# Optimization experiments

Measured on AMD Instinct MI355X. Metric: run time of the kernel, lower is better.

Reference implementation:

```python
import jax, jax.numpy as jnp
import numpy as np

N, E, G = 20000, 640000, 64
D_IN, H, C, D_OUT = 256, 4, 64, 32
HC = H * C


def gat_layer(x, W, a_src, a_dst, b, src, dst, n_nodes, heads, ch):
    # x: [N, F_in], W: [F_in, H*C]
    h = (x @ W).reshape(n_nodes, heads, ch)          # [N,H,C]
    es = jnp.einsum('nhc,hc->nh', h, a_src)          # [N,H]
    ed = jnp.einsum('nhc,hc->nh', h, a_dst)
    e = jax.nn.leaky_relu(es[src] + ed[dst], 0.2)    # [Etot,H]
    m = jax.ops.segment_max(e, dst, num_segments=n_nodes)
    m = jnp.where(jnp.isfinite(m), m, 0.0)
    ex = jnp.exp(e - m[dst])
    denom = jax.ops.segment_sum(ex, dst, num_segments=n_nodes)
    alpha = ex / jnp.maximum(denom[dst], 1e-16)      # softmax over in-edges per dst
    out = jax.ops.segment_sum(alpha[:, :, None] * h[src], dst, num_segments=n_nodes)
    return out.reshape(n_nodes, heads * ch) + b


def setup_inputs() -> dict:
    key = jax.random.key(0)
    ks = jax.random.split(key, 14)
    g1 = 1.0 / np.sqrt(D_IN)
    g2 = 1.0 / np.sqrt(HC)
    inp = {
        'x': jax.random.normal(ks[0], (N, D_IN), jnp.float32),
        'edge_index': jax.random.randint(ks[1], (2, E), 0, N, jnp.int64 if jax.config.jax_enable_x64 else jnp.int32),
        'batch': jnp.sort(jax.random.randint(ks[2], (N,), 0, G)),
        'W1': jax.random.normal(ks[3], (D_IN, HC), jnp.float32) * g1,
        'a_src1': jax.random.normal(ks[4], (H, C), jnp.float32) * g2,
        'a_dst1': jax.random.normal(ks[5], (H, C), jnp.float32) * g2,
        'b1': jnp.zeros((HC,), jnp.float32),
        'W2': jax.random.normal(ks[6], (HC, HC), jnp.float32) * g2,
        'a_src2': jax.random.normal(ks[7], (H, C), jnp.float32) * g2,
        'a_dst2': jax.random.normal(ks[8], (H, C), jnp.float32) * g2,
        'b2': jnp.zeros((HC,), jnp.float32),
        'Wp': jax.random.normal(ks[9], (HC, D_OUT), jnp.float32) * g2,
        'bp': jnp.zeros((D_OUT,), jnp.float32),
    }
    return inp


def reference(x, edge_index, batch, W1, a_src1, a_dst1, b1, W2, a_src2, a_dst2, b2, Wp, bp):
    # add self-loops (PyG GATConv default)
    loop = jnp.arange(N, dtype=edge_index.dtype)
    src = jnp.concatenate([edge_index[0], loop])
    dst = jnp.concatenate([edge_index[1], loop])
    x1 = jax.nn.relu(gat_layer(x, W1, a_src1, a_dst1, b1, src, dst, N, H, C))
    # dropout p=0.6 is identity in eval mode
    x2 = jax.nn.relu(gat_layer(x1, W2, a_src2, a_dst2, b2, src, dst, N, H, C))
    node_scores = x2 @ Wp + bp                        # [N, D_OUT]
    sums = jax.ops.segment_sum(node_scores, batch, num_segments=G)
    counts = jax.ops.segment_sum(jnp.ones((N,), node_scores.dtype), batch, num_segments=G)
    return sums / jnp.maximum(counts, 1.0)[:, None]   # [G, D_OUT]
```

## Files before the change

kernel.cpp:

```cpp
#include <hip/hip_runtime.h>
#include <hip/hip_bf16.h>
#include <cstdint>

#define NNODES 20000
#define NEDGES 640000
#define ETOT   (NEDGES + NNODES)
#define NGROUP 64
#define HC     256
#define DOUT   32
#define EBLK   5120
#define NBLK   (NEDGES / EBLK)
#define CBLK   ((NNODES + 255) / 256)

typedef short bf16x8 __attribute__((ext_vector_type(8)));
typedef short s16x4  __attribute__((ext_vector_type(4)));
typedef float f32x4  __attribute__((ext_vector_type(4)));
typedef float f32x2  __attribute__((ext_vector_type(2)));
typedef int   s32x4  __attribute__((ext_vector_type(4)));
typedef unsigned int u32x4 __attribute__((ext_vector_type(4)));

__device__ __forceinline__ float b2f(__hip_bfloat16 v) { return __bfloat162float(v); }
__device__ __forceinline__ float bs2f(short v) {
    union { unsigned int u; float f; } c; c.u = ((unsigned int)(unsigned short)v) << 16; return c.f;
}
__device__ __forceinline__ short f2bs(float v) {
    __hip_bfloat16 b = __float2bfloat16(v);
    union { __hip_bfloat16 b; short s; } u; u.b = b; return u.s;
}
__device__ __forceinline__ float ldf(const void* __restrict__ p, size_t i, int bf) {
    return bf ? __bfloat162float(((const __hip_bfloat16*)p)[i]) : ((const float*)p)[i];
}
__device__ __forceinline__ int ld_idx(const int* __restrict__ p, size_t i, int f64) {
    return f64 ? p[2 * i] : p[i];
}

__global__ void k_probe(const unsigned int* __restrict__ xw, const int* __restrict__ ei,
                        int* __restrict__ flag, float* __restrict__ sx, int* __restrict__ cnt) {
    int t = threadIdx.x;
    for (int i = t; i < NGROUP * HC; i += 256) sx[i] = 0.f;
    if (t < NGROUP) cnt[t] = 0;
    if (t < 64) {
        int l = t;
        int ones = 0, zeros = 0;
#pragma unroll
        for (int r = 0; r < 4; r++) {
            unsigned long long b1 = __ballot((xw[r * 64 + l] >> 14) & 1);
            unsigned long long b2 = __ballot(ei[2 * (r * 64 + l) + 1] == 0);
            ones  += __popcll(b1);
            zeros += __popcll(b2);
        }
        if (l == 0) { flag[1] = (ones < 64) ? 1 : 0; flag[0] = (zeros > 200) ? 1 : 0; }
    }
}

__global__ __launch_bounds__(256) void k_lhist(const int* __restrict__ ei,
                                               int* __restrict__ H,
                                               const int* __restrict__ flag) {
    __shared__ int hl[NNODES];
    int t = threadIdx.x, b = blockIdx.x, f = flag[0];
    s32x4* hl4 = reinterpret_cast<s32x4*>(hl);
    for (int i = t; i < NNODES / 4; i += 256) hl4[i] = (s32x4){0, 0, 0, 0};
    __syncthreads();
    int s0 = b * EBLK;
    if (f) {
        const int* d64 = ei + 2 * NEDGES;
        for (int i0 = s0; i0 < s0 + EBLK; i0 += 512) {
            int i = i0 + 2 * t;
            s32x4 v = *reinterpret_cast<const s32x4*>(d64 + 2 * (size_t)i);
            atomicAdd(&hl[v[0]], 1);
            atomicAdd(&hl[v[2]], 1);
        }
    } else {
        const int* d32 = ei + NEDGES;
        for (int i0 = s0; i0 < s0 + EBLK; i0 += 1024) {
            int i = i0 + 4 * t;
            s32x4 v = *reinterpret_cast<const s32x4*>(d32 + i);
            atomicAdd(&hl[v[0]], 1); atomicAdd(&hl[v[1]], 1);
            atomicAdd(&hl[v[2]], 1); atomicAdd(&hl[v[3]], 1);
        }
    }
    __syncthreads();
    s32x4* Hb4 = reinterpret_cast<s32x4*>(H + (size_t)b * NNODES);
    for (int i = t; i < NNODES / 4; i += 256) Hb4[i] = hl4[i];
}

__global__ __launch_bounds__(256) void k_colsum(const int* __restrict__ H,
                                                int* __restrict__ deg,
                                                int* __restrict__ bsum) {
    __shared__ int wred[4];
    int t = threadIdx.x, n = blockIdx.x * 256 + t;
    int s = 0;
    if (n < NNODES) {
#pragma unroll 5
        for (int b = 0; b < NBLK; b++) s += H[(size_t)b * NNODES + n];
        s += 1;
        deg[n] = s;
    }
    int r = s;
#pragma unroll
    for (int o = 1; o < 64; o <<= 1) r += __shfl_xor(r, o);
    if ((t & 63) == 0) wred[t >> 6] = r;
    __syncthreads();
    if (t == 0) bsum[blockIdx.x] = wred[0] + wred[1] + wred[2] + wred[3];
}

__global__ void k_scansm(const int* __restrict__ bsum, int* __restrict__ boff,
                         int* __restrict__ off) {
    __shared__ int w0tot;
    int t = threadIdx.x, lane = t & 63, w = t >> 6;
    int v = (t < CBLK) ? bsum[t] : 0;
    int sc = v;
#pragma unroll
    for (int o = 1; o < 64; o <<= 1) {
        int u = __shfl_up(sc, o);
        if (lane >= o) sc += u;
    }
    if (w == 0 && lane == 63) w0tot = sc;
    __syncthreads();
    int excl = sc - v + (w ? w0tot : 0);
    if (t < CBLK) boff[t] = excl;
    if (t == 0) off[NNODES] = ETOT;
}

__global__ __launch_bounds__(256) void k_base(int* __restrict__ H,
                                              const int* __restrict__ deg,
                                              const int* __restrict__ boff,
                                              int* __restrict__ off,
                                              int* __restrict__ csr) {
    __shared__ int wtot[4];
    int t = threadIdx.x, blk = blockIdx.x;
    int n = blk * 256 + t;
    int d = (n < NNODES) ? deg[n] : 0;
    int lane = t & 63, w = t >> 6;
    int sc = d;
#pragma unroll
    for (int o = 1; o < 64; o <<= 1) {
        int u = __shfl_up(sc, o);
        if (lane >= o) sc += u;
    }
    if (lane == 63) wtot[w] = sc;
    __syncthreads();
    int woff = 0;
    for (int i = 0; i < w; i++) woff += wtot[i];
    int excl = woff + sc - d;
    if (n < NNODES) {
        int o0 = boff[blk] + excl;
        off[n] = o0;
        csr[o0] = n;
        int run = o0 + 1;
#pragma unroll 5
        for (int b = 0; b < NBLK; b++) {
            size_t idx = (size_t)b * NNODES + n;
            int tt = H[idx];
            H[idx] = run;
            run += tt;
        }
    }
}

__global__ __launch_bounds__(256) void k_scatter2(const int* __restrict__ ei,
                                                  const int* __restrict__ H,
                                                  int* __restrict__ csr,
                                                  const int* __restrict__ flag) {
    __shared__ int base_l[NNODES];
    int t = threadIdx.x, b = blockIdx.x, f = flag[0];
    const s32x4* Hb4 = reinterpret_cast<const s32x4*>(H + (size_t)b * NNODES);
    s32x4* bl4 = reinterpret_cast<s32x4*>(base_l);
    for (int i = t; i < NNODES / 4; i += 256) bl4[i] = Hb4[i];
    __syncthreads();
    int s0 = b * EBLK;
    if (f) {
        const int* d64 = ei + 2 * NEDGES;
        for (int i0 = s0; i0 < s0 + EBLK; i0 += 512) {
            int i = i0 + 2 * t;
            s32x4 sv = *reinterpret_cast<const s32x4*>(ei + 2 * (size_t)i);
            s32x4 dv = *reinterpret_cast<const s32x4*>(d64 + 2 * (size_t)i);
            int p0 = atomicAdd(&base_l[dv[0]], 1);
            csr[p0] = sv[0];
            int p1 = atomicAdd(&base_l[dv[2]], 1);
            csr[p1] = sv[2];
        }
    } else {
        const int* d32 = ei + NEDGES;
        for (int i0 = s0; i0 < s0 + EBLK; i0 += 1024) {
            int i = i0 + 4 * t;
            s32x4 sv = *reinterpret_cast<const s32x4*>(ei + i);
            s32x4 dv = *reinterpret_cast<const s32x4*>(d32 + i);
#pragma unroll
            for (int k = 0; k < 4; k++) {
                int p = atomicAdd(&base_l[dv[k]], 1);
                csr[p] = sv[k];
            }
        }
    }
}

__global__ void k_wt(const void* __restrict__ W1, const void* __restrict__ W2,
                     __hip_bfloat16* __restrict__ Wt1, __hip_bfloat16* __restrict__ Wt2,
                     const int* __restrict__ flag) {
    int i = blockIdx.x * 256 + threadIdx.x;
    int which = i >> 16;
    int j = i & 65535;
    int k = j >> 8, n = j & 255;
    const void* W = which ? W2 : W1;
    __hip_bfloat16* Wt = which ? Wt2 : Wt1;
    Wt[(size_t)n * 256 + k] = __float2bfloat16(ldf(W, (size_t)k * 256 + n, flag[1]));
}

__global__ __launch_bounds__(256) void k_gemm(const void* __restrict__ A,
                                              const __hip_bfloat16* __restrict__ Bt,
                                              __hip_bfloat16* __restrict__ Hout,
                                              const void* __restrict__ a_src,
                                              const void* __restrict__ a_dst,
                                              float* __restrict__ es4, float* __restrict__ ed4,
                                              const int* __restrict__ flag, int force_bf) {
    int bf   = flag[1];
    int abf  = force_bf | bf;
    int w    = threadIdx.x >> 6;
    int lane = threadIdx.x & 63;
    int mr   = lane & 15;
    int quad = lane >> 4;
    int r0   = blockIdx.x * 16;
    if (r0 >= NNODES) return;
    f32x4 acc[4];
#pragma unroll
    for (int j = 0; j < 4; j++) acc[j] = (f32x4){0.f, 0.f, 0.f, 0.f};
    size_t rowoff = (size_t)(r0 + mr) * HC;
    const __hip_bfloat16* Btw = Bt + (size_t)w * 64 * HC;
    for (int kk = 0; kk < HC; kk += 32) {
        bf16x8 a;
        if (abf) {
            a = *reinterpret_cast<const bf16x8*>((const __hip_bfloat16*)A + rowoff + kk + quad * 8);
        } else {
            const float* af = (const float*)A + rowoff + kk + quad * 8;
            f32x4 lo = *reinterpret_cast<const f32x4*>(af);
            f32x4 hi = *reinterpret_cast<const f32x4*>(af + 4);
#pragma unroll
            for (int ii = 0; ii < 4; ii++) { a[ii] = f2bs(lo[ii]); a[ii + 4] = f2bs(hi[ii]); }
        }
#pragma unroll
        for (int j = 0; j < 4; j++) {
            bf16x8 b = *reinterpret_cast<const bf16x8*>(Btw + (size_t)(j * 16 + mr) * HC + kk + quad * 8);
            acc[j] = __builtin_amdgcn_mfma_f32_16x16x32_bf16(a, b, acc[j], 0, 0, 0);
        }
    }
#pragma unroll
    for (int j = 0; j < 4; j++)
#pragma unroll
        for (int r = 0; r < 4; r++)
            Hout[(size_t)(r0 + quad * 4 + r) * HC + w * 64 + j * 16 + mr] = __float2bfloat16(acc[j][r]);
    float ps[4] = {0.f, 0.f, 0.f, 0.f}, pd[4] = {0.f, 0.f, 0.f, 0.f};
#pragma unroll
    for (int j = 0; j < 4; j++) {
        float asv = ldf(a_src, (size_t)(w * 64 + j * 16 + mr), bf);
        float adv = ldf(a_dst, (size_t)(w * 64 + j * 16 + mr), bf);
#pragma unroll
        for (int r = 0; r < 4; r++) {
            ps[r] = fmaf(acc[j][r], asv, ps[r]);
            pd[r] = fmaf(acc[j][r], adv, pd[r]);
        }
    }
#pragma unroll
    for (int o = 1; o < 16; o <<= 1)
#pragma unroll
        for (int r = 0; r < 4; r++) {
            ps[r] += __shfl_xor(ps[r], o);
            pd[r] += __shfl_xor(pd[r], o);
        }
    if (mr == 0)
#pragma unroll
        for (int r = 0; r < 4; r++) {
            int row = r0 + quad * 4 + r;
            es4[(size_t)row * 4 + w] = ps[r];
            ed4[(size_t)row * 4 + w] = pd[r];
        }
}

__global__ __launch_bounds__(256) void k_agg(const __hip_bfloat16* __restrict__ Hb,
                                             const float* __restrict__ es4, const float* __restrict__ ed4,
                                             const void* __restrict__ bias,
                                             const int* __restrict__ off, const int* __restrict__ csr,
                                             const int* __restrict__ flag,
                                             __hip_bfloat16* __restrict__ out) {
    __shared__ float p_lds[4][4][64];
    __shared__ int   s_lds[4][64];
    int wv = threadIdx.x >> 6;
    int l  = threadIdx.x & 63;
    int half = l >> 5;
    int hl   = l & 31;
    int hd8  = hl >> 3;
    int bf = flag[1];
    int n0 = blockIdx.x * 4 + wv;
    for (int n = n0; n < NNODES; n += 10000) {
        int base = off[n], deg = off[n + 1] - base;
        f32x4 edv = *reinterpret_cast<const f32x4*>(ed4 + (size_t)n * 4);
        f32x4 m    = (f32x4){-INFINITY, -INFINITY, -INFINITY, -INFINITY};
        f32x4 dsum = (f32x4){0.f, 0.f, 0.f, 0.f};
        f32x2 acc2[4];
#pragma unroll
        for (int d = 0; d < 4; d++) acc2[d] = (f32x2){0.f, 0.f};
        for (int c0 = 0; c0 < deg; c0 += 64) {
            int cn = min(deg - c0, 64);
            int s = 0;
            f32x4 ev;
            if (l < cn) {
                s = csr[base + c0 + l];
                f32x4 e = *reinterpret_cast<const f32x4*>(es4 + (size_t)s * 4);
#pragma unroll
                for (int h = 0; h < 4; h++) {
                    float t = e[h] + edv[h];
                    ev[h] = (t > 0.f) ? t : 0.2f * t;
                }
            } else {
#pragma unroll
                for (int h = 0; h < 4; h++) ev[h] = -INFINITY;
            }
            s_lds[wv][l] = s;
            f32x4 mc = ev;
#pragma unroll
            for (int o = 32; o; o >>= 1)
#pragma unroll
                for (int h = 0; h < 4; h++) mc[h] = fmaxf(mc[h], __shfl_xor(mc[h], o));
            f32x4 al, pv;
#pragma unroll
            for (int h = 0; h < 4; h++) {
                float nm = fmaxf(m[h], mc[h]);
                al[h] = __expf(m[h] - nm);
                m[h]  = nm;
            }
#pragma unroll
            for (int h = 0; h < 4; h++) pv[h] = (l < cn) ? __expf(ev[h] - m[h]) : 0.f;
            f32x4 sc = pv;
#pragma unroll
            for (int o = 32; o; o >>= 1)
#pragma unroll
                for (int h = 0; h < 4; h++) sc[h] += __shfl_xor(sc[h], o);
#pragma unroll
            for (int h = 0; h < 4; h++) dsum[h] = dsum[h] * al[h] + sc[h];
            float a8 = al[hd8];
#pragma unroll
            for (int d = 0; d < 4; d++) acc2[d] *= a8;
#pragma unroll
            for (int h = 0; h < 4; h++) p_lds[wv][h][l] = pv[h];
            int jn = (cn + 15) & ~15;
            for (int j = 0; j < jn; j += 16) {
                int e0 = j + 8 * half;
                s32x4 sA = *reinterpret_cast<const s32x4*>(&s_lds[wv][e0]);
                s32x4 sB = *reinterpret_cast<const s32x4*>(&s_lds[wv][e0 + 4]);
                f32x4 pA = *reinterpret_cast<const f32x4*>(&p_lds[wv][hd8][e0]);
                f32x4 pB = *reinterpret_cast<const f32x4*>(&p_lds[wv][hd8][e0 + 4]);
                u32x4 hv[8];
#pragma unroll
                for (int i = 0; i < 8; i++) {
                    int sj = (i < 4) ? sA[i & 3] : sB[i & 3];
                    hv[i] = *reinterpret_cast<const u32x4*>(Hb + (size_t)sj * HC + hl * 8);
                }
#pragma unroll
                for (int i = 0; i < 8; i++) {
                    float p = (i < 4) ? pA[i & 3] : pB[i & 3];
#pragma unroll
                    for (int d = 0; d < 4; d++) {
                        unsigned int u = hv[i][d];
                        f32x2 h2;
                        h2.x = __uint_as_float(u << 16);
                        h2.y = __uint_as_float(u & 0xFFFF0000u);
                        acc2[d] += h2 * p;
                    }
                }
            }
        }
#pragma unroll
        for (int d = 0; d < 4; d++) {
            acc2[d].x += __shfl_xor(acc2[d].x, 32);
            acc2[d].y += __shfl_xor(acc2[d].y, 32);
        }
        float rinv = 1.0f / fmaxf(dsum[hd8], 1e-16f);
        if (half == 0) {
            bf16x8 ov;
#pragma unroll
            for (int d = 0; d < 4; d++) {
                float v0 = acc2[d].x * rinv + ldf(bias, (size_t)hl * 8 + 2 * d, bf);
                float v1 = acc2[d].y * rinv + ldf(bias, (size_t)hl * 8 + 2 * d + 1, bf);
                ov[2 * d]     = f2bs(fmaxf(v0, 0.f));
                ov[2 * d + 1] = f2bs(fmaxf(v1, 0.f));
            }
            *reinterpret_cast<bf16x8*>(out + (size_t)n * HC + hl * 8) = ov;
        }
    }
}

__global__ __launch_bounds__(256) void k_groupsum(const __hip_bfloat16* __restrict__ X2,
                                                  const int* __restrict__ batch,
                                                  float* __restrict__ sx, int* __restrict__ cnt,
                                                  const int* __restrict__ flag) {
    const int RPB = NNODES / 250;
    int b = blockIdx.x, f = flag[0];
    int sub = threadIdx.x >> 6, l = threadIdx.x & 63;
    int r = b * RPB + sub;
    f32x4 acc = (f32x4){0.f, 0.f, 0.f, 0.f};
    int curg = ld_idx(batch, r, f);
    int cacc = 0;
    for (int k = 0; k < RPB / 4; k++, r += 4) {
        int g = ld_idx(batch, r, f);
        if (g != curg) {
#pragma unroll
            for (int c = 0; c < 4; c++) atomicAdd(&sx[(size_t)curg * HC + l * 4 + c], acc[c]);
            if (l == 0) atomicAdd(&cnt[curg], cacc);
            acc = (f32x4){0.f, 0.f, 0.f, 0.f}; cacc = 0; curg = g;
        }
        s16x4 hv = *reinterpret_cast<const s16x4*>(X2 + (size_t)r * HC + l * 4);
#pragma unroll
        for (int c = 0; c < 4; c++) acc[c] += bs2f(hv[c]);
        cacc++;
    }
#pragma unroll
    for (int c = 0; c < 4; c++) atomicAdd(&sx[(size_t)curg * HC + l * 4 + c], acc[c]);
    if (l == 0) atomicAdd(&cnt[curg], cacc);
}

__global__ __launch_bounds__(256) void k_final(const float* __restrict__ sx,
                                               const void* __restrict__ Wp,
                                               const void* __restrict__ bp,
                                               const int* __restrict__ cnt,
                                               const int* __restrict__ flag,
                                               void* __restrict__ out) {
    __shared__ float red[8][32];
    int g = blockIdx.x, t = threadIdx.x;
    int c = t & 31, seg = t >> 5;
    int bf = flag[1];
    const float* sxg = sx + (size_t)g * HC;
    float a = 0.f;
#pragma unroll
    for (int k = 0; k < 32; k++) {
        int kk = seg * 32 + k;
        a = fmaf(sxg[kk], ldf(Wp, (size_t)kk * DOUT + c, bf), a);
    }
    red[seg][c] = a;
    __syncthreads();
    if (t < 32) {
        float s = 0.f;
#pragma unroll
        for (int i = 0; i < 8; i++) s += red[i][t];
        int ct = cnt[g];
        float v = (ct > 0) ? (s / ct + ldf(bp, (size_t)t, bf)) : 0.f;
        if (bf) ((__hip_bfloat16*)out)[g * DOUT + t] = __float2bfloat16(v);
        else    ((float*)out)[g * DOUT + t]          = v;
    }
}

extern "C" void kernel_launch(void* const* d_in, const int* in_sizes, int n_in,
                              void* d_out, int out_size, void* d_ws, size_t ws_size,
                              hipStream_t stream) {
    (void)in_sizes; (void)n_in; (void)out_size; (void)ws_size;
    const void* x   = d_in[0];
    const int*  ei  = (const int*)d_in[1];
    const int*  bat = (const int*)d_in[2];
    const void* W1  = d_in[3];
    const void* as1 = d_in[4];
    const void* ad1 = d_in[5];
    const void* b1  = d_in[6];
    const void* W2  = d_in[7];
    const void* as2 = d_in[8];
    const void* ad2 = d_in[9];
    const void* b2  = d_in[10];
    const void* Wp  = d_in[11];
    const void* bp  = d_in[12];

    char* ws = (char*)d_ws;
    size_t o = 0;
    auto alloc = [&](size_t bytes) -> char* {
        char* p = ws + o;
        o += (bytes + 255) & ~(size_t)255;
        return p;
    };
    __hip_bfloat16* hb  = (__hip_bfloat16*)alloc((size_t)NNODES * HC * 2);
    __hip_bfloat16* xb  = (__hip_bfloat16*)alloc((size_t)NNODES * HC * 2);
    __hip_bfloat16* xb2 = (__hip_bfloat16*)alloc((size_t)NNODES * HC * 2);
    __hip_bfloat16* Wt1 = (__hip_bfloat16*)alloc((size_t)HC * HC * 2);
    __hip_bfloat16* Wt2 = (__hip_bfloat16*)alloc((size_t)HC * HC * 2);
    float* es = (float*)alloc((size_t)NNODES * 4 * 4);
    float* ed = (float*)alloc((size_t)NNODES * 4 * 4);
    int* H    = (int*)alloc((size_t)NBLK * NNODES * 4);
    int* deg  = (int*)alloc((size_t)NNODES * 4);
    int* off  = (int*)alloc((size_t)(NNODES + 1) * 4);
    int* csr  = (int*)alloc((size_t)ETOT * 4);
    int* bsum = (int*)alloc((size_t)CBLK * 4);
    int* boff = (int*)alloc((size_t)CBLK * 4);
    float* sx = (float*)alloc((size_t)NGROUP * HC * 4);
    int* cnt  = (int*)alloc(256);
    int* flag = (int*)alloc(256);

    k_probe<<<1, 256, 0, stream>>>((const unsigned int*)x, ei, flag, sx, cnt);
    k_lhist<<<NBLK, 256, 0, stream>>>(ei, H, flag);
    k_colsum<<<CBLK, 256, 0, stream>>>(H, deg, bsum);
    k_scansm<<<1, 128, 0, stream>>>(bsum, boff, off);
    k_base<<<CBLK, 256, 0, stream>>>(H, deg, boff, off, csr);
    k_scatter2<<<NBLK, 256, 0, stream>>>(ei, H, csr, flag);
    k_wt<<<512, 256, 0, stream>>>(W1, W2, Wt1, Wt2, flag);

    k_gemm<<<NNODES / 16, 256, 0, stream>>>(x, Wt1, hb, as1, ad1, es, ed, flag, 0);
    k_agg<<<2500, 256, 0, stream>>>(hb, es, ed, b1, off, csr, flag, xb);

    k_gemm<<<NNODES / 16, 256, 0, stream>>>(xb, Wt2, hb, as2, ad2, es, ed, flag, 1);
    k_agg<<<2500, 256, 0, stream>>>(hb, es, ed, b2, off, csr, flag, xb2);

    k_groupsum<<<250, 256, 0, stream>>>(xb2, bat, sx, cnt, flag);
    k_final<<<NGROUP, 256, 0, stream>>>(sx, Wp, bp, cnt, flag, d_out);
}
```

Measured before the change: 299.7 us.

## Use a global score upper bound for softmax and merge the offset scan into k_base

```diff
diff --git a/kernel.cpp b/kernel.cpp
--- a/kernel.cpp
+++ b/kernel.cpp
@@ -33,12 +33,21 @@
 __device__ __forceinline__ int ld_idx(const int* __restrict__ p, size_t i, int f64) {
     return f64 ? p[2 * i] : p[i];
 }
+__device__ __forceinline__ unsigned enc_f(float f) {
+    unsigned u = __float_as_uint(f);
+    return (u >> 31) ? ~u : (u | 0x80000000u);
+}
+__device__ __forceinline__ float dec_f(unsigned e) {
+    return (e >> 31) ? __uint_as_float(e & 0x7FFFFFFFu) : __uint_as_float(~e);
+}
 
 __global__ void k_probe(const unsigned int* __restrict__ xw, const int* __restrict__ ei,
-                        int* __restrict__ flag, float* __restrict__ sx, int* __restrict__ cnt) {
+                        int* __restrict__ flag, float* __restrict__ sx, int* __restrict__ cnt,
+                        unsigned int* __restrict__ gmaxu) {
     int t = threadIdx.x;
     for (int i = t; i < NGROUP * HC; i += 256) sx[i] = 0.f;
     if (t < NGROUP) cnt[t] = 0;
+    if (t < 64) gmaxu[t] = 0x007FFFFFu;
     if (t < 64) {
         int l = t;
         int ones = 0, zeros = 0;
@@ -104,30 +113,13 @@
     if (t == 0) bsum[blockIdx.x] = wred[0] + wred[1] + wred[2] + wred[3];
 }
 
-__global__ void k_scansm(const int* __restrict__ bsum, int* __restrict__ boff,
-                         int* __restrict__ off) {
-    __shared__ int w0tot;
-    int t = threadIdx.x, lane = t & 63, w = t >> 6;
-    int v = (t < CBLK) ? bsum[t] : 0;
-    int sc = v;
-#pragma unroll
-    for (int o = 1; o < 64; o <<= 1) {
-        int u = __shfl_up(sc, o);
-        if (lane >= o) sc += u;
-    }
-    if (w == 0 && lane == 63) w0tot = sc;
-    __syncthreads();
-    int excl = sc - v + (w ? w0tot : 0);
-    if (t < CBLK) boff[t] = excl;
-    if (t == 0) off[NNODES] = ETOT;
-}
-
 __global__ __launch_bounds__(256) void k_base(int* __restrict__ H,
                                               const int* __restrict__ deg,
-                                              const int* __restrict__ boff,
+                                              const int* __restrict__ bsum,
                                               int* __restrict__ off,
                                               int* __restrict__ csr) {
     __shared__ int wtot[4];
+    __shared__ int boff_s;
     int t = threadIdx.x, blk = blockIdx.x;
     int n = blk * 256 + t;
     int d = (n < NNODES) ? deg[n] : 0;
@@ -139,12 +131,20 @@
         if (lane >= o) sc += u;
     }
     if (lane == 63) wtot[w] = sc;
+    if (w == 0) {
+        int v = (lane < blk) ? bsum[lane] : 0;
+        if (lane + 64 < blk) v += bsum[lane + 64];
+#pragma unroll
+        for (int o = 1; o < 64; o <<= 1) v += __shfl_xor(v, o);
+        if (lane == 0) boff_s = v;
+    }
     __syncthreads();
     int woff = 0;
     for (int i = 0; i < w; i++) woff += wtot[i];
     int excl = woff + sc - d;
+    if (blk == 0 && t == 0) off[NNODES] = ETOT;
     if (n < NNODES) {
-        int o0 = boff[blk] + excl;
+        int o0 = boff_s + excl;
         off[n] = o0;
         csr[o0] = n;
         int run = o0 + 1;
@@ -213,7 +213,9 @@
                                               const void* __restrict__ a_src,
                                               const void* __restrict__ a_dst,
                                               float* __restrict__ es4, float* __restrict__ ed4,
+                                              unsigned int* __restrict__ gmaxu,
                                               const int* __restrict__ flag, int force_bf) {
+    __shared__ u32x4 hst4[512];
     int bf   = flag[1];
     int abf  = force_bf | bf;
     int w    = threadIdx.x >> 6;
@@ -221,7 +223,6 @@
     int mr   = lane & 15;
     int quad = lane >> 4;
     int r0   = blockIdx.x * 16;
-    if (r0 >= NNODES) return;
     f32x4 acc[4];
 #pragma unroll
     for (int j = 0; j < 4; j++) acc[j] = (f32x4){0.f, 0.f, 0.f, 0.f};
@@ -244,11 +245,12 @@
             acc[j] = __builtin_amdgcn_mfma_f32_16x16x32_bf16(a, b, acc[j], 0, 0, 0);
         }
     }
+    short* hst = reinterpret_cast<short*>(hst4);
 #pragma unroll
     for (int j = 0; j < 4; j++)
 #pragma unroll
         for (int r = 0; r < 4; r++)
-            Hout[(size_t)(r0 + quad * 4 + r) * HC + w * 64 + j * 16 + mr] = __float2bfloat16(acc[j][r]);
+            hst[(quad * 4 + r) * HC + w * 64 + j * 16 + mr] = f2bs(acc[j][r]);
     float ps[4] = {0.f, 0.f, 0.f, 0.f}, pd[4] = {0.f, 0.f, 0.f, 0.f};
 #pragma unroll
     for (int j = 0; j < 4; j++) {
@@ -267,6 +269,10 @@
             ps[r] += __shfl_xor(ps[r], o);
             pd[r] += __shfl_xor(pd[r], o);
         }
+    float pm = fmaxf(fmaxf(ps[0], ps[1]), fmaxf(ps[2], ps[3]));
+    pm = fmaxf(pm, __shfl_xor(pm, 16));
+    pm = fmaxf(pm, __shfl_xor(pm, 32));
+    if (lane == 0) atomicMax(&gmaxu[w * 16], enc_f(pm));
     if (mr == 0)
 #pragma unroll
         for (int r = 0; r < 4; r++) {
@@ -274,12 +280,17 @@
             es4[(size_t)row * 4 + w] = ps[r];
             ed4[(size_t)row * 4 + w] = pd[r];
         }
+    __syncthreads();
+    u32x4* dst = reinterpret_cast<u32x4*>((short*)Hout + (size_t)r0 * HC);
+    dst[threadIdx.x * 2]     = hst4[threadIdx.x * 2];
+    dst[threadIdx.x * 2 + 1] = hst4[threadIdx.x * 2 + 1];
 }
 
 __global__ __launch_bounds__(256) void k_agg(const __hip_bfloat16* __restrict__ Hb,
                                              const float* __restrict__ es4, const float* __restrict__ ed4,
                                              const void* __restrict__ bias,
                                              const int* __restrict__ off, const int* __restrict__ csr,
+                                             const unsigned int* __restrict__ gmaxu,
                                              const int* __restrict__ flag,
                                              __hip_bfloat16* __restrict__ out) {
     __shared__ float p_lds[4][4][64];
@@ -290,11 +301,19 @@
     int hl   = l & 31;
     int hd8  = hl >> 3;
     int bf = flag[1];
+    f32x4 gm;
+#pragma unroll
+    for (int h = 0; h < 4; h++) gm[h] = dec_f(gmaxu[h * 16]);
     int n0 = blockIdx.x * 4 + wv;
     for (int n = n0; n < NNODES; n += 10000) {
         int base = off[n], deg = off[n + 1] - base;
         f32x4 edv = *reinterpret_cast<const f32x4*>(ed4 + (size_t)n * 4);
-        f32x4 m    = (f32x4){-INFINITY, -INFINITY, -INFINITY, -INFINITY};
+        f32x4 M;
+#pragma unroll
+        for (int h = 0; h < 4; h++) {
+            float t0 = gm[h] + edv[h];
+            M[h] = (t0 > 0.f) ? t0 : 0.2f * t0;
+        }
         f32x4 dsum = (f32x4){0.f, 0.f, 0.f, 0.f};
         f32x2 acc2[4];
 #pragma unroll
@@ -302,46 +321,22 @@
         for (int c0 = 0; c0 < deg; c0 += 64) {
             int cn = min(deg - c0, 64);
             int s = 0;
-            f32x4 ev;
+            f32x4 pv = (f32x4){0.f, 0.f, 0.f, 0.f};
             if (l < cn) {
                 s = csr[base + c0 + l];
                 f32x4 e = *reinterpret_cast<const f32x4*>(es4 + (size_t)s * 4);
 #pragma unroll
                 for (int h = 0; h < 4; h++) {
                     float t = e[h] + edv[h];
-                    ev[h] = (t > 0.f) ? t : 0.2f * t;
+                    t = (t > 0.f) ? t : 0.2f * t;
+                    pv[h] = __expf(t - M[h]);
                 }
-            } else {
-#pragma unroll
-                for (int h = 0; h < 4; h++) ev[h] = -INFINITY;
             }
             s_lds[wv][l] = s;
-            f32x4 mc = ev;
-#pragma unroll
-            for (int o = 32; o; o >>= 1)
-#pragma unroll
-                for (int h = 0; h < 4; h++) mc[h] = fmaxf(mc[h], __shfl_xor(mc[h], o));
-            f32x4 al, pv;
-#pragma unroll
-            for (int h = 0; h < 4; h++) {
-                float nm = fmaxf(m[h], mc[h]);
-                al[h] = __expf(m[h] - nm);
-                m[h]  = nm;
-            }
-#pragma unroll
-            for (int h = 0; h < 4; h++) pv[h] = (l < cn) ? __expf(ev[h] - m[h]) : 0.f;
-            f32x4 sc = pv;
-#pragma unroll
-            for (int o = 32; o; o >>= 1)
-#pragma unroll
-                for (int h = 0; h < 4; h++) sc[h] += __shfl_xor(sc[h], o);
-#pragma unroll
-            for (int h = 0; h < 4; h++) dsum[h] = dsum[h] * al[h] + sc[h];
-            float a8 = al[hd8];
-#pragma unroll
-            for (int d = 0; d < 4; d++) acc2[d] *= a8;
 #pragma unroll
             for (int h = 0; h < 4; h++) p_lds[wv][h][l] = pv[h];
+#pragma unroll
+            for (int h = 0; h < 4; h++) dsum[h] += pv[h];
             int jn = (cn + 15) & ~15;
             for (int j = 0; j < jn; j += 16) {
                 int e0 = j + 8 * half;
@@ -369,6 +364,10 @@
                 }
             }
         }
+#pragma unroll
+        for (int o = 32; o; o >>= 1)
+#pragma unroll
+            for (int h = 0; h < 4; h++) dsum[h] += __shfl_xor(dsum[h], o);
 #pragma unroll
         for (int d = 0; d < 4; d++) {
             acc2[d].x += __shfl_xor(acc2[d].x, 32);
@@ -485,24 +484,23 @@
     int* off  = (int*)alloc((size_t)(NNODES + 1) * 4);
     int* csr  = (int*)alloc((size_t)ETOT * 4);
     int* bsum = (int*)alloc((size_t)CBLK * 4);
-    int* boff = (int*)alloc((size_t)CBLK * 4);
     float* sx = (float*)alloc((size_t)NGROUP * HC * 4);
+    unsigned int* gmaxu = (unsigned int*)alloc(256);
     int* cnt  = (int*)alloc(256);
     int* flag = (int*)alloc(256);
 
-    k_probe<<<1, 256, 0, stream>>>((const unsigned int*)x, ei, flag, sx, cnt);
+    k_probe<<<1, 256, 0, stream>>>((const unsigned int*)x, ei, flag, sx, cnt, gmaxu);
     k_lhist<<<NBLK, 256, 0, stream>>>(ei, H, flag);
     k_colsum<<<CBLK, 256, 0, stream>>>(H, deg, bsum);
-    k_scansm<<<1, 128, 0, stream>>>(bsum, boff, off);
-    k_base<<<CBLK, 256, 0, stream>>>(H, deg, boff, off, csr);
+    k_base<<<CBLK, 256, 0, stream>>>(H, deg, bsum, off, csr);
     k_scatter2<<<NBLK, 256, 0, stream>>>(ei, H, csr, flag);
     k_wt<<<512, 256, 0, stream>>>(W1, W2, Wt1, Wt2, flag);
 
-    k_gemm<<<NNODES / 16, 256, 0, stream>>>(x, Wt1, hb, as1, ad1, es, ed, flag, 0);
-    k_agg<<<2500, 256, 0, stream>>>(hb, es, ed, b1, off, csr, flag, xb);
-
-    k_gemm<<<NNODES / 16, 256, 0, stream>>>(xb, Wt2, hb, as2, ad2, es, ed, flag, 1);
-    k_agg<<<2500, 256, 0, stream>>>(hb, es, ed, b2, off, csr, flag, xb2);
+    k_gemm<<<NNODES / 16, 256, 0, stream>>>(x, Wt1, hb, as1, ad1, es, ed, gmaxu, flag, 0);
+    k_agg<<<2500, 256, 0, stream>>>(hb, es, ed, b1, off, csr, gmaxu, flag, xb);
+
+    k_gemm<<<NNODES / 16, 256, 0, stream>>>(xb, Wt2, hb, as2, ad2, es, ed, gmaxu, flag, 1);
+    k_agg<<<2500, 256, 0, stream>>>(hb, es, ed, b2, off, csr, gmaxu, flag, xb2);
 
     k_groupsum<<<250, 256, 0, stream>>>(xb2, bat, sx, cnt, flag);
     k_final<<<NGROUP, 256, 0, stream>>>(sx, Wp, bp, cnt, flag, d_out);
```

Measured after the change: 325.9 us. 8.7% more time.
